# Kernel optimization log

Measured on AMD Instinct MI355X. Metric: run time of the kernel, lower is better.

## Reference

```python
import jax, jax.numpy as jnp
import numpy as np

M_LOCAL = 100000
N_GLOBAL = 50000
C = 128
E = 1600000
EDGE_DIM = 16
BN_EPS = 1e-5


def setup_inputs() -> dict:
    key = jax.random.key(0)
    ks = jax.random.split(key, 12)
    s = 1.0 / np.sqrt(C)
    inp = {
        "h_local": jax.random.normal(ks[0], (M_LOCAL, C), jnp.float32),
        "h_global": jax.random.normal(ks[1], (N_GLOBAL, C), jnp.float32),
        "ea_flat": jax.random.normal(ks[2], (E, EDGE_DIM), jnp.float32),
        # GIN MLP: Linear(C,C) -> ReLU -> Linear(C,C)
        "W1": jax.random.normal(ks[3], (C, C), jnp.float32) * s,
        "b1": jnp.zeros((C,), jnp.float32),
        "W2": jax.random.normal(ks[4], (C, C), jnp.float32) * s,
        "b2": jnp.zeros((C,), jnp.float32),
        "eps": jnp.zeros((), jnp.float32),  # GIN train_eps, init 0
        "gamma_l": jnp.ones((C,), jnp.float32),
        "beta_l": jnp.zeros((C,), jnp.float32),
        "gamma_g": jnp.ones((C,), jnp.float32),
        "beta_g": jnp.zeros((C,), jnp.float32),
        "intra_ei": jax.random.randint(ks[5], (2, E), 0, M_LOCAL, jnp.int32),
        "node_ids": jax.random.randint(ks[6], (M_LOCAL,), 0, N_GLOBAL, jnp.int32),
        "valid": jnp.ones((M_LOCAL,), jnp.bool_),
        "N_total": N_GLOBAL,
    }
    return inp


def _batchnorm(x, gamma, beta):
    # training-mode BN: biased batch statistics over node dim
    mu = jnp.mean(x, axis=0)
    var = jnp.mean((x - mu) ** 2, axis=0)
    return (x - mu) * jax.lax.rsqrt(var + BN_EPS) * gamma + beta


def reference(h_local, h_global, ea_flat, W1, b1, W2, b2, eps,
              gamma_l, beta_l, gamma_g, beta_g,
              intra_ei, node_ids, valid, N_total):
    M = h_local.shape[0]
    valid_f = valid.astype(h_local.dtype)[:, None]
    clamped = jnp.maximum(node_ids, 0)

    # inject global context, zero padding
    h_in = (h_local + h_global[clamped]) * valid_f

    # GINConv: mlp((1+eps)*x + sum_{j->i} x_j)   (ea_flat unused for 'gin')
    src, dst = intra_ei[0], intra_ei[1]
    agg = jax.ops.segment_sum(h_in[src], dst, num_segments=M)
    pre = (1.0 + eps) * h_in + agg
    h_local_new = jnp.maximum(pre @ W1 + b1, 0.0) @ W2 + b2
    h_local_new = h_local_new * valid_f

    # cross-subgraph consensus: scatter mean into global nodes
    h_sum = jax.ops.segment_sum(h_local_new, clamped, num_segments=N_total)
    v_cnt = jax.ops.segment_sum(valid_f[:, 0], clamped, num_segments=N_total)
    h_global_new = h_sum / jnp.maximum(v_cnt, 1.0)[:, None]

    # local track: BN + residual (Identity since in==out) + mask (dropout p=0)
    h_local_new = _batchnorm(h_local_new, gamma_l, beta_l) + h_local
    h_local_new = h_local_new * valid_f

    # global track: BN + residual
    h_global_new = _batchnorm(h_global_new, gamma_g, beta_g) + h_global

    return (h_local_new, h_global_new)
```

## Files before the change

kernel.cpp:

```cpp
#include <hip/hip_runtime.h>

#define CDIM 128
#define BROWS 128
#define HROWS 64
#define SMAX2 2048
#define CHUNK 16384
#define PBLK 1024

typedef __bf16 bf16x8 __attribute__((ext_vector_type(8)));
typedef __bf16 bf16x4 __attribute__((ext_vector_type(4)));
typedef float f32x4 __attribute__((ext_vector_type(4)));

__global__ __launch_bounds__(256) void k_init(
    const float* __restrict__ hl, const float* __restrict__ hg,
    const int* __restrict__ nid, __bf16* __restrict__ h_in, int M)
{
    int idx = blockIdx.x * 256 + threadIdx.x;
    if (idx >= M * 16) return;
    int i = idx >> 4, q8 = idx & 15;
    int g = max(nid[i], 0);
    const float4* hl4 = reinterpret_cast<const float4*>(hl);
    const float4* hg4 = reinterpret_cast<const float4*>(hg);
    float4 a0 = hl4[i * 32 + q8 * 2], a1 = hl4[i * 32 + q8 * 2 + 1];
    float4 b0 = hg4[g * 32 + q8 * 2], b1 = hg4[g * 32 + q8 * 2 + 1];
    bf16x8 o;
    o[0] = (__bf16)(a0.x + b0.x); o[1] = (__bf16)(a0.y + b0.y);
    o[2] = (__bf16)(a0.z + b0.z); o[3] = (__bf16)(a0.w + b0.w);
    o[4] = (__bf16)(a1.x + b1.x); o[5] = (__bf16)(a1.y + b1.y);
    o[6] = (__bf16)(a1.z + b1.z); o[7] = (__bf16)(a1.w + b1.w);
    *reinterpret_cast<bf16x8*>(&h_in[(size_t)i * CDIM + q8 * 8]) = o;
}

__global__ __launch_bounds__(256) void k_count(
    const int* __restrict__ ei, const int* __restrict__ nid,
    int* __restrict__ bcnt, int* __restrict__ deg_g, int E, int M)
{
    __shared__ int lh[1024];
    int t = threadIdx.x;
    for (int i = t; i < 1024; i += 256) lh[i] = 0;
    __syncthreads();
    int stride = gridDim.x * 256;
    for (int e = blockIdx.x * 256 + t; e < E; e += stride)
        atomicAdd(&lh[ei[E + e] >> 7], 1);
    for (int i = blockIdx.x * 256 + t; i < M; i += stride)
        atomicAdd(&deg_g[max(nid[i], 0)], 1);
    __syncthreads();
    for (int i = t; i < 1024; i += 256)
        if (lh[i]) atomicAdd(&bcnt[i], lh[i]);
}

__global__ __launch_bounds__(1024) void k_scanA(
    const int* __restrict__ deg_g, int* __restrict__ bsum_g, int N, int nbN,
    const int* __restrict__ bcnt, int* __restrict__ bboff,
    int* __restrict__ bcur, int NB)
{
    __shared__ int sh[1024];
    int t = threadIdx.x;
    if ((int)blockIdx.x < nbN) {
        int i = blockIdx.x * 1024 + t;
        sh[t] = (i < N) ? deg_g[i] : 0;
        __syncthreads();
        for (int s = 512; s > 0; s >>= 1) {
            if (t < s) sh[t] += sh[t + s];
            __syncthreads();
        }
        if (t == 0) bsum_g[blockIdx.x] = sh[0];
    } else {
        int v = (t < NB) ? bcnt[t] : 0;
        sh[t] = v;
        __syncthreads();
        for (int s = 1; s < 1024; s <<= 1) {
            int a = (t >= s) ? sh[t - s] : 0;
            __syncthreads();
            sh[t] += a;
            __syncthreads();
        }
        if (t < NB) { int ex = sh[t] - v; bboff[t] = ex; bcur[t] = ex; }
        if (t == 0) bboff[NB] = sh[1023];
    }
}

__global__ __launch_bounds__(256) void k_scanB(int* __restrict__ bsum, int nb)
{
    __shared__ int sh[256];
    int t = threadIdx.x;
    int v = (t < nb) ? bsum[t] : 0;
    sh[t] = v;
    __syncthreads();
    for (int s = 1; s < 256; s <<= 1) {
        int a = (t >= s) ? sh[t - s] : 0;
        __syncthreads();
        sh[t] += a;
        __syncthreads();
    }
    if (t < nb) bsum[t] = sh[t] - v;
}

__global__ __launch_bounds__(1024) void k_scanC(
    const int* __restrict__ deg_g, const int* __restrict__ bsum_g,
    int* __restrict__ off_g, int N)
{
    __shared__ int sh[1024];
    int i = blockIdx.x * 1024 + threadIdx.x;
    int v = (i < N) ? deg_g[i] : 0;
    sh[threadIdx.x] = v;
    __syncthreads();
    for (int s = 1; s < 1024; s <<= 1) {
        int a = (threadIdx.x >= (unsigned)s) ? sh[threadIdx.x - s] : 0;
        __syncthreads();
        sh[threadIdx.x] += a;
        __syncthreads();
    }
    if (i < N) off_g[i] = bsum_g[blockIdx.x] + sh[threadIdx.x] - v;
}

__global__ __launch_bounds__(256) void k_bscatter(
    const int* __restrict__ ei, const int* __restrict__ nid,
    int* __restrict__ bcur, int* __restrict__ packed,
    const int* __restrict__ off_g, int* __restrict__ cur_g,
    int* __restrict__ rows_g, int E, int M)
{
    __shared__ int lh[1024];
    int t = threadIdx.x;
    int e0 = blockIdx.x * CHUNK;
    int n = min(CHUNK, E - e0);
    for (int i = t; i < 1024; i += 256) lh[i] = 0;
    __syncthreads();
    for (int j = t; j < n; j += 256)
        atomicAdd(&lh[ei[E + e0 + j] >> 7], 1);
    __syncthreads();
    for (int i = t; i < 1024; i += 256) {
        int c = lh[i];
        if (c) lh[i] = atomicAdd(&bcur[i], c);
    }
    __syncthreads();
    for (int j = t; j < n; j += 256) {
        int s = ei[e0 + j], d = ei[E + e0 + j];
        int pos = atomicAdd(&lh[d >> 7], 1);
        packed[pos] = s | ((d & 127) << 17);
    }
    for (int i = blockIdx.x * 256 + t; i < M; i += gridDim.x * 256) {
        int g = max(nid[i], 0);
        int pos = off_g[g] + atomicAdd(&cur_g[g], 1);
        rows_g[pos] = i;
    }
}

__global__ __launch_bounds__(256) void k_agg_fused(
    const __bf16* __restrict__ h_in, const int* __restrict__ packed,
    const int* __restrict__ bboff, const float* __restrict__ epsp,
    __bf16* __restrict__ pre, int M)
{
    __shared__ int lsrc[SMAX2];
    __shared__ int lcnt[HROWS], lbase[HROWS], lpos[HROWS];
    int t = threadIdx.x;
    int b = blockIdx.x >> 1;
    int half = blockIdx.x & 1;
    int base = bboff[b];
    int n = bboff[b + 1] - base;
    if (t < HROWS) lcnt[t] = 0;
    __syncthreads();
    for (int j = t; j < n; j += 256) {
        int ld = packed[base + j] >> 17;
        if ((ld >> 6) == half) atomicAdd(&lcnt[ld & 63], 1);
    }
    __syncthreads();
    int v = (t < HROWS) ? lcnt[t] : 0;
    if (t < HROWS) lbase[t] = v;
    __syncthreads();
    for (int s = 1; s < HROWS; s <<= 1) {
        int a = (t < HROWS && t >= s) ? lbase[t - s] : 0;
        __syncthreads();
        if (t < HROWS) lbase[t] += a;
        __syncthreads();
    }
    if (t < HROWS) { lbase[t] -= v; lpos[t] = lbase[t]; }
    __syncthreads();
    for (int j = t; j < n; j += 256) {
        int p = packed[base + j];
        int ld = p >> 17;
        if ((ld >> 6) == half) {
            int r = atomicAdd(&lpos[ld & 63], 1);
            if (r < SMAX2) lsrc[r] = p & 0x1FFFF;
        }
    }
    __syncthreads();

    float es = 1.0f + epsp[0];
    int slot = t >> 4, q = t & 15;
    int r0 = b * BROWS + half * HROWS;
    for (int rr = slot; rr < HROWS; rr += 16) {
        int row = r0 + rr;
        if (row >= M) break;
        bf16x8 a = *reinterpret_cast<const bf16x8*>(&h_in[(size_t)row * CDIM + q * 8]);
        float f[8];
#pragma unroll
        for (int k2 = 0; k2 < 8; ++k2) f[k2] = es * (float)a[k2];
        int sb = lbase[rr], cnt = lcnt[rr];
        for (int j = 0; j < cnt; ++j) {
            int s = lsrc[sb + j];
            bf16x8 vv = *reinterpret_cast<const bf16x8*>(&h_in[(size_t)s * CDIM + q * 8]);
#pragma unroll
            for (int k2 = 0; k2 < 8; ++k2) f[k2] += (float)vv[k2];
        }
        bf16x8 o;
#pragma unroll
        for (int k2 = 0; k2 < 8; ++k2) o[k2] = (__bf16)f[k2];
        *reinterpret_cast<bf16x8*>(&pre[(size_t)row * CDIM + q * 8]) = o;
    }
}

__global__ __launch_bounds__(256) void k_wprep(
    const float* __restrict__ W1, const float* __restrict__ W2,
    __bf16* __restrict__ Wt1, __bf16* __restrict__ Wt2)
{
    int idx = blockIdx.x * 256 + threadIdx.x;
    int k = idx >> 7, n = idx & 127;
    Wt1[n * CDIM + k] = (__bf16)W1[k * CDIM + n];
    Wt2[n * CDIM + k] = (__bf16)W2[k * CDIM + n];
}

template <int RELU>
__global__ __launch_bounds__(256) void k_gemm_mfma(
    const __bf16* __restrict__ A, const __bf16* __restrict__ Wt,
    const float* __restrict__ bias, __bf16* __restrict__ out, int M)
{
    __shared__ bf16x8 w_lds4[2048];
    int t = threadIdx.x;
#pragma unroll
    for (int j = 0; j < 8; ++j) {
        int c = t + j * 256;
        int n = c >> 4;
        int cr = c & 15;
        int kc = cr >> 2;
        int g = cr & 3;
        int dest = ((n >> 4) * 4 + kc) * 64 + g * 16 + (n & 15);
        w_lds4[dest] = reinterpret_cast<const bf16x8*>(Wt)[c];
    }
    __syncthreads();

    int wave = t >> 6, lane = t & 63;
    int r0 = blockIdx.x * 64 + wave * 16;
    int arow = r0 + (lane & 15);
    int srcrow = min(arow, M - 1);
    int krow = (lane >> 4) * 8;

    bf16x8 a[4];
#pragma unroll
    for (int kc = 0; kc < 4; ++kc)
        a[kc] = *reinterpret_cast<const bf16x8*>(
            &A[(size_t)srcrow * CDIM + kc * 32 + krow]);

    f32x4 acc[8] = {};
#pragma unroll
    for (int kc = 0; kc < 4; ++kc) {
#pragma unroll
        for (int nt = 0; nt < 8; ++nt) {
            bf16x8 b = w_lds4[(nt * 4 + kc) * 64 + lane];
            acc[nt] = __builtin_amdgcn_mfma_f32_16x16x32_bf16(a[kc], b, acc[nt], 0, 0, 0);
        }
    }

    int col = lane & 15;
    int rowbase = r0 + (lane >> 4) * 4;
#pragma unroll
    for (int nt = 0; nt < 8; ++nt) {
        float bv = bias[nt * 16 + col];
#pragma unroll
        for (int reg = 0; reg < 4; ++reg) {
            int row = rowbase + reg;
            if (row >= M) continue;
            float v = acc[nt][reg] + bv;
            if (RELU) v = fmaxf(v, 0.f);
            out[(size_t)row * CDIM + nt * 16 + col] = (__bf16)v;
        }
    }
}

__global__ __launch_bounds__(256) void k_gmean(
    const __bf16* __restrict__ y, const int* __restrict__ off,
    const int* __restrict__ deg, const int* __restrict__ rows,
    float* __restrict__ out_g, float* __restrict__ part, int N)
{
    int t = threadIdx.x;
    int q = t & 31;
    float4 csum = make_float4(0.f, 0.f, 0.f, 0.f);
    float4 csq  = make_float4(0.f, 0.f, 0.f, 0.f);
    for (int g = blockIdx.x * 8 + (t >> 5); g < N; g += gridDim.x * 8) {
        int s0 = off[g], n = deg[g];
        float4 acc = make_float4(0.f, 0.f, 0.f, 0.f);
        for (int j = 0; j < n; ++j) {
            int r = rows[s0 + j];
            bf16x4 v = *reinterpret_cast<const bf16x4*>(&y[(size_t)r * CDIM + q * 4]);
            acc.x += (float)v[0]; acc.y += (float)v[1];
            acc.z += (float)v[2]; acc.w += (float)v[3];
        }
        float inv = 1.0f / fmaxf((float)n, 1.0f);
        float4 m = make_float4(acc.x * inv, acc.y * inv, acc.z * inv, acc.w * inv);
        reinterpret_cast<float4*>(out_g)[(size_t)g * 32 + q] = m;
        csum.x += m.x; csum.y += m.y; csum.z += m.z; csum.w += m.w;
        csq.x = fmaf(m.x, m.x, csq.x); csq.y = fmaf(m.y, m.y, csq.y);
        csq.z = fmaf(m.z, m.z, csq.z); csq.w = fmaf(m.w, m.w, csq.w);
    }
    __shared__ float4 red[256];
    float* pb = part + (size_t)blockIdx.x * 256;
    red[t] = csum;
    __syncthreads();
    if (t < 32) {
        float4 a = red[t];
#pragma unroll
        for (int g = 1; g < 8; ++g) {
            float4 b = red[g * 32 + t];
            a.x += b.x; a.y += b.y; a.z += b.z; a.w += b.w;
        }
        reinterpret_cast<float4*>(pb)[t] = a;
    }
    __syncthreads();
    red[t] = csq;
    __syncthreads();
    if (t < 32) {
        float4 a = red[t];
#pragma unroll
        for (int g = 1; g < 8; ++g) {
            float4 b = red[g * 32 + t];
            a.x += b.x; a.y += b.y; a.z += b.z; a.w += b.w;
        }
        reinterpret_cast<float4*>(pb + 128)[t] = a;
    }
}

__global__ __launch_bounds__(256) void k_stats_y(
    const __bf16* __restrict__ y, float* __restrict__ part, int M)
{
    int t = threadIdx.x;
    int q = t & 31;
    float4 csum = make_float4(0.f, 0.f, 0.f, 0.f);
    float4 csq  = make_float4(0.f, 0.f, 0.f, 0.f);
    for (int p = blockIdx.x * 8 + (t >> 5); p < M; p += gridDim.x * 8) {
        bf16x4 v = *reinterpret_cast<const bf16x4*>(&y[(size_t)p * CDIM + q * 4]);
        float a = (float)v[0], b = (float)v[1], c = (float)v[2], d = (float)v[3];
        csum.x += a; csum.y += b; csum.z += c; csum.w += d;
        csq.x = fmaf(a, a, csq.x); csq.y = fmaf(b, b, csq.y);
        csq.z = fmaf(c, c, csq.z); csq.w = fmaf(d, d, csq.w);
    }
    __shared__ float4 red[256];
    float* pb = part + (size_t)blockIdx.x * 256;
    red[t] = csum;
    __syncthreads();
    if (t < 32) {
        float4 a = red[t];
#pragma unroll
        for (int g = 1; g < 8; ++g) {
            float4 b = red[g * 32 + t];
            a.x += b.x; a.y += b.y; a.z += b.z; a.w += b.w;
        }
        reinterpret_cast<float4*>(pb)[t] = a;
    }
    __syncthreads();
    red[t] = csq;
    __syncthreads();
    if (t < 32) {
        float4 a = red[t];
#pragma unroll
        for (int g = 1; g < 8; ++g) {
            float4 b = red[g * 32 + t];
            a.x += b.x; a.y += b.y; a.z += b.z; a.w += b.w;
        }
        reinterpret_cast<float4*>(pb + 128)[t] = a;
    }
}

__global__ __launch_bounds__(256) void k_reduce(
    const float* __restrict__ part_l, const float* __restrict__ part_g,
    float* __restrict__ stats)
{
    int r = blockIdx.x;
    const float* part = (r < 256) ? part_l : part_g;
    int col = r & 255;
    int t = threadIdx.x;
    float s = 0.f;
#pragma unroll
    for (int j = 0; j < PBLK / 256; ++j)
        s += part[(size_t)(t + j * 256) * 256 + col];
    __shared__ float sh[256];
    sh[t] = s;
    __syncthreads();
    for (int w = 128; w > 0; w >>= 1) {
        if (t < w) sh[t] += sh[t + w];
        __syncthreads();
    }
    if (t == 0) stats[(r < 256 ? 0 : 256) + col] = sh[0];
}

__global__ void k_scale(
    const float* __restrict__ stats, const float* __restrict__ gl,
    const float* __restrict__ bl, const float* __restrict__ gg,
    const float* __restrict__ bg, float* __restrict__ sc, int M, int N)
{
    int t = threadIdx.x;
    if (t < 128) {
        float invM = 1.0f / (float)M;
        float mu = stats[t] * invM;
        float var = stats[128 + t] * invM - mu * mu;
        float s = gl[t] * rsqrtf(var + 1e-5f);
        sc[t] = s;
        sc[128 + t] = bl[t] - mu * s;
    } else if (t < 256) {
        int c = t - 128;
        float invN = 1.0f / (float)N;
        float mu = stats[256 + c] * invN;
        float var = stats[384 + c] * invN - mu * mu;
        float s = gg[c] * rsqrtf(var + 1e-5f);
        sc[256 + c] = s;
        sc[384 + c] = bg[c] - mu * s;
    }
}

__global__ __launch_bounds__(256) void k_fin_l(
    const __bf16* __restrict__ y, const float* __restrict__ res,
    const float* __restrict__ sc, float* __restrict__ out_l, int M)
{
    int idx = blockIdx.x * 256 + threadIdx.x;
    if (idx >= M * 32) return;
    int q = idx & 31;
    float4 s4 = reinterpret_cast<const float4*>(sc)[q];
    float4 h4 = reinterpret_cast<const float4*>(sc + 128)[q];
    bf16x4 v = *reinterpret_cast<const bf16x4*>(&y[(size_t)idx * 4]);
    float4 r = reinterpret_cast<const float4*>(res)[idx];
    reinterpret_cast<float4*>(out_l)[idx] = make_float4(
        fmaf((float)v[0], s4.x, h4.x) + r.x, fmaf((float)v[1], s4.y, h4.y) + r.y,
        fmaf((float)v[2], s4.z, h4.z) + r.z, fmaf((float)v[3], s4.w, h4.w) + r.w);
}

__global__ __launch_bounds__(256) void k_fin_g(
    float* __restrict__ X, const float* __restrict__ res,
    const float* __restrict__ sc, int rows)
{
    int idx = blockIdx.x * 256 + threadIdx.x;
    if (idx >= rows * 32) return;
    int q = idx & 31;
    float4 s4 = reinterpret_cast<const float4*>(sc)[q];
    float4 h4 = reinterpret_cast<const float4*>(sc + 128)[q];
    float4 v = reinterpret_cast<float4*>(X)[idx];
    float4 r = reinterpret_cast<const float4*>(res)[idx];
    reinterpret_cast<float4*>(X)[idx] = make_float4(
        fmaf(v.x, s4.x, h4.x) + r.x, fmaf(v.y, s4.y, h4.y) + r.y,
        fmaf(v.z, s4.z, h4.z) + r.z, fmaf(v.w, s4.w, h4.w) + r.w);
}

extern "C" void kernel_launch(void* const* d_in, const int* in_sizes, int n_in,
                              void* d_out, int out_size, void* d_ws, size_t ws_size,
                              hipStream_t stream)
{
    const float* h_local  = (const float*)d_in[0];
    const float* h_global = (const float*)d_in[1];
    const float* W1   = (const float*)d_in[3];
    const float* b1   = (const float*)d_in[4];
    const float* W2   = (const float*)d_in[5];
    const float* b2   = (const float*)d_in[6];
    const float* eps  = (const float*)d_in[7];
    const float* gl   = (const float*)d_in[8];
    const float* bl   = (const float*)d_in[9];
    const float* gg   = (const float*)d_in[10];
    const float* bg   = (const float*)d_in[11];
    const int*   ei   = (const int*)d_in[12];
    const int*   nid  = (const int*)d_in[13];

    const int M = in_sizes[13];
    const int N = in_sizes[1] / CDIM;
    const int E = in_sizes[12] / 2;
    const int NB = (M + BROWS - 1) / BROWS;

    float* out_l = (float*)d_out;
    float* out_g = out_l + (size_t)M * CDIM;

    __bf16* pre = (__bf16*)d_out;

    int* deg_g  = (int*)((char*)d_out + 26000000);
    int* cur_g  = deg_g + N;
    int* off_g  = cur_g + N;
    int* rows_g = off_g + N;
    int* bsum_g = rows_g + M;

    float* part_l = (float*)((char*)d_out + 28000000);
    float* part_g = part_l + (size_t)PBLK * 256;

    int* packed = (int*)out_g;

    __bf16* h_in = (__bf16*)d_ws;
    __bf16* h1   = h_in;
    __bf16* y    = (__bf16*)((char*)d_ws + 25600000);
    char*  wst   = (char*)d_ws + 51200000;
    __bf16* Wt1  = (__bf16*)wst;
    __bf16* Wt2  = Wt1 + CDIM * CDIM;
    int*   bcnt  = (int*)(Wt2 + CDIM * CDIM);
    int*   bboff = bcnt + 1024;
    int*   bcur  = bboff + 1024;
    float* stats = (float*)(bcur + 1024);
    float* sc    = stats + 512;

    const int nbN = (N + 1023) / 1024;

    hipMemsetAsync(deg_g, 0, (size_t)2 * N * sizeof(int), stream);
    hipMemsetAsync(bcnt, 0, 1024 * sizeof(int), stream);

    k_wprep<<<64, 256, 0, stream>>>(W1, W2, Wt1, Wt2);

    int gInit = (M * 16 + 255) / 256;
    k_init<<<gInit, 256, 0, stream>>>(h_local, h_global, nid, h_in, M);

    k_count<<<256, 256, 0, stream>>>(ei, nid, bcnt, deg_g, E, M);
    k_scanA<<<nbN + 1, 1024, 0, stream>>>(deg_g, bsum_g, N, nbN, bcnt, bboff, bcur, NB);
    k_scanB<<<1, 256, 0, stream>>>(bsum_g, nbN);
    k_scanC<<<nbN, 1024, 0, stream>>>(deg_g, bsum_g, off_g, N);

    int gBS = (E + CHUNK - 1) / CHUNK;
    k_bscatter<<<gBS, 256, 0, stream>>>(ei, nid, bcur, packed,
                                        off_g, cur_g, rows_g, E, M);

    k_agg_fused<<<NB * 2, 256, 0, stream>>>(h_in, packed, bboff, eps, pre, M);

    int gGemm = (M + 63) / 64;
    k_gemm_mfma<1><<<gGemm, 256, 0, stream>>>(pre, Wt1, b1, h1, M);
    k_gemm_mfma<0><<<gGemm, 256, 0, stream>>>(h1, Wt2, b2, y, M);

    k_gmean<<<PBLK, 256, 0, stream>>>(y, off_g, deg_g, rows_g, out_g, part_g, N);
    k_stats_y<<<PBLK, 256, 0, stream>>>(y, part_l, M);
    k_reduce<<<512, 256, 0, stream>>>(part_l, part_g, stats);

    k_scale<<<1, 256, 0, stream>>>(stats, gl, bl, gg, bg, sc, M, N);

    int gFinL = (M * 32 + 255) / 256;
    k_fin_l<<<gFinL, 256, 0, stream>>>(y, h_local, sc, out_l, M);
    int gFinG = (N * 32 + 255) / 256;
    k_fin_g<<<gFinG, 256, 0, stream>>>(out_g, h_global, sc + 256, N);
}
```

Baseline: 275.0 us.

## Fuse both MLP GEMMs and BN statistics into one kernel, split aggregation finer

The two MFMA GEMM launches become a single k_mlp kernel. The ReLU'd hidden tile stays in LDS and the second weight matrix is reloaded into the same LDS buffer. Per-column sum and sum-of-squares for the local BatchNorm are gathered in the GEMM epilogue through shuffles and LDS atomics, which removes the separate k_stats_y pass over y and the global round trip of h1. The neighbour aggregation now splits each 128-row bucket into quarters instead of halves, with a smaller LDS source list, and unrolls the gather loop by two. The gmean grid is also enlarged. Risks: the smaller per-quarter LDS list (1024) could overflow on high-degree buckets, and the fused kernel's larger LDS footprint may lower occupancy.

```diff
diff --git a/kernel.cpp b/kernel.cpp
--- a/kernel.cpp
+++ b/kernel.cpp
@@ -2,10 +2,11 @@
 
 #define CDIM 128
 #define BROWS 128
-#define HROWS 64
-#define SMAX2 2048
+#define QROWS 32
+#define SMAXQ 1024
 #define CHUNK 16384
-#define PBLK 1024
+#define GMB 2048
+#define H1LD 136
 
 typedef __bf16 bf16x8 __attribute__((ext_vector_type(8)));
 typedef __bf16 bf16x4 __attribute__((ext_vector_type(4)));
@@ -151,45 +152,47 @@
     const int* __restrict__ bboff, const float* __restrict__ epsp,
     __bf16* __restrict__ pre, int M)
 {
-    __shared__ int lsrc[SMAX2];
-    __shared__ int lcnt[HROWS], lbase[HROWS], lpos[HROWS];
-    int t = threadIdx.x;
-    int b = blockIdx.x >> 1;
-    int half = blockIdx.x & 1;
+    __shared__ int lsrc[SMAXQ];
+    __shared__ int lcnt[QROWS], lbase[QROWS], lpos[QROWS];
+    int t = threadIdx.x;
+    int b = blockIdx.x >> 2;
+    int quarter = blockIdx.x & 3;
     int base = bboff[b];
     int n = bboff[b + 1] - base;
-    if (t < HROWS) lcnt[t] = 0;
+    if (t < QROWS) lcnt[t] = 0;
     __syncthreads();
     for (int j = t; j < n; j += 256) {
         int ld = packed[base + j] >> 17;
-        if ((ld >> 6) == half) atomicAdd(&lcnt[ld & 63], 1);
-    }
-    __syncthreads();
-    int v = (t < HROWS) ? lcnt[t] : 0;
-    if (t < HROWS) lbase[t] = v;
-    __syncthreads();
-    for (int s = 1; s < HROWS; s <<= 1) {
-        int a = (t < HROWS && t >= s) ? lbase[t - s] : 0;
-        __syncthreads();
-        if (t < HROWS) lbase[t] += a;
-        __syncthreads();
-    }
-    if (t < HROWS) { lbase[t] -= v; lpos[t] = lbase[t]; }
+        if ((ld >> 5) == quarter) atomicAdd(&lcnt[ld & 31], 1);
+    }
+    __syncthreads();
+    int v = (t < QROWS) ? lcnt[t] : 0;
+    if (t < QROWS) lbase[t] = v;
+    __syncthreads();
+    for (int s = 1; s < QROWS; s <<= 1) {
+        int a = (t < QROWS && t >= s) ? lbase[t - s] : 0;
+        __syncthreads();
+        if (t < QROWS) lbase[t] += a;
+        __syncthreads();
+    }
+    if (t < QROWS) { lbase[t] -= v; lpos[t] = lbase[t]; }
     __syncthreads();
     for (int j = t; j < n; j += 256) {
         int p = packed[base + j];
         int ld = p >> 17;
-        if ((ld >> 6) == half) {
-            int r = atomicAdd(&lpos[ld & 63], 1);
-            if (r < SMAX2) lsrc[r] = p & 0x1FFFF;
+        if ((ld >> 5) == quarter) {
+            int r = atomicAdd(&lpos[ld & 31], 1);
+            if (r < SMAXQ) lsrc[r] = p & 0x1FFFF;
         }
     }
     __syncthreads();
 
     float es = 1.0f + epsp[0];
     int slot = t >> 4, q = t & 15;
-    int r0 = b * BROWS + half * HROWS;
-    for (int rr = slot; rr < HROWS; rr += 16) {
+    int r0 = b * BROWS + quarter * QROWS;
+#pragma unroll
+    for (int rr0 = 0; rr0 < 2; ++rr0) {
+        int rr = slot + rr0 * 16;
         int row = r0 + rr;
         if (row >= M) break;
         bf16x8 a = *reinterpret_cast<const bf16x8*>(&h_in[(size_t)row * CDIM + q * 8]);
@@ -197,11 +200,19 @@
 #pragma unroll
         for (int k2 = 0; k2 < 8; ++k2) f[k2] = es * (float)a[k2];
         int sb = lbase[rr], cnt = lcnt[rr];
-        for (int j = 0; j < cnt; ++j) {
-            int s = lsrc[sb + j];
-            bf16x8 vv = *reinterpret_cast<const bf16x8*>(&h_in[(size_t)s * CDIM + q * 8]);
-#pragma unroll
-            for (int k2 = 0; k2 < 8; ++k2) f[k2] += (float)vv[k2];
+        int j = 0;
+        for (; j + 1 < cnt; j += 2) {
+            int s0 = lsrc[sb + j], s1 = lsrc[sb + j + 1];
+            bf16x8 v0 = *reinterpret_cast<const bf16x8*>(&h_in[(size_t)s0 * CDIM + q * 8]);
+            bf16x8 v1 = *reinterpret_cast<const bf16x8*>(&h_in[(size_t)s1 * CDIM + q * 8]);
+#pragma unroll
+            for (int k2 = 0; k2 < 8; ++k2) f[k2] += (float)v0[k2] + (float)v1[k2];
+        }
+        if (j < cnt) {
+            int s0 = lsrc[sb + j];
+            bf16x8 v0 = *reinterpret_cast<const bf16x8*>(&h_in[(size_t)s0 * CDIM + q * 8]);
+#pragma unroll
+            for (int k2 = 0; k2 < 8; ++k2) f[k2] += (float)v0[k2];
         }
         bf16x8 o;
 #pragma unroll
@@ -220,61 +231,105 @@
     Wt2[n * CDIM + k] = (__bf16)W2[k * CDIM + n];
 }
 
-template <int RELU>
-__global__ __launch_bounds__(256) void k_gemm_mfma(
-    const __bf16* __restrict__ A, const __bf16* __restrict__ Wt,
-    const float* __restrict__ bias, __bf16* __restrict__ out, int M)
+__global__ __launch_bounds__(256) void k_mlp(
+    const __bf16* __restrict__ pre, const __bf16* __restrict__ Wt1,
+    const __bf16* __restrict__ Wt2, const float* __restrict__ b1,
+    const float* __restrict__ b2, __bf16* __restrict__ y,
+    float* __restrict__ part, int M)
 {
     __shared__ bf16x8 w_lds4[2048];
+    __shared__ __bf16 h1t[64 * H1LD];
+    __shared__ float pst[256];
     int t = threadIdx.x;
 #pragma unroll
     for (int j = 0; j < 8; ++j) {
         int c = t + j * 256;
-        int n = c >> 4;
-        int cr = c & 15;
-        int kc = cr >> 2;
-        int g = cr & 3;
-        int dest = ((n >> 4) * 4 + kc) * 64 + g * 16 + (n & 15);
-        w_lds4[dest] = reinterpret_cast<const bf16x8*>(Wt)[c];
-    }
+        int n = c >> 4, cr = c & 15, kc = cr >> 2, g = cr & 3;
+        w_lds4[((n >> 4) * 4 + kc) * 64 + g * 16 + (n & 15)] =
+            reinterpret_cast<const bf16x8*>(Wt1)[c];
+    }
+    if (t < 256) pst[t] = 0.f;
     __syncthreads();
 
     int wave = t >> 6, lane = t & 63;
     int r0 = blockIdx.x * 64 + wave * 16;
-    int arow = r0 + (lane & 15);
-    int srcrow = min(arow, M - 1);
+    int srcrow = min(r0 + (lane & 15), M - 1);
     int krow = (lane >> 4) * 8;
+    int col = lane & 15;
 
     bf16x8 a[4];
 #pragma unroll
     for (int kc = 0; kc < 4; ++kc)
         a[kc] = *reinterpret_cast<const bf16x8*>(
-            &A[(size_t)srcrow * CDIM + kc * 32 + krow]);
-
-    f32x4 acc[8] = {};
-#pragma unroll
-    for (int kc = 0; kc < 4; ++kc) {
-#pragma unroll
-        for (int nt = 0; nt < 8; ++nt) {
-            bf16x8 b = w_lds4[(nt * 4 + kc) * 64 + lane];
-            acc[nt] = __builtin_amdgcn_mfma_f32_16x16x32_bf16(a[kc], b, acc[nt], 0, 0, 0);
-        }
-    }
-
-    int col = lane & 15;
+            &pre[(size_t)srcrow * CDIM + kc * 32 + krow]);
+
+    f32x4 acc1[8] = {};
+#pragma unroll
+    for (int kc = 0; kc < 4; ++kc)
+#pragma unroll
+        for (int nt = 0; nt < 8; ++nt)
+            acc1[nt] = __builtin_amdgcn_mfma_f32_16x16x32_bf16(
+                a[kc], w_lds4[(nt * 4 + kc) * 64 + lane], acc1[nt], 0, 0, 0);
+
+    int lrowb = wave * 16 + (lane >> 4) * 4;
+#pragma unroll
+    for (int nt = 0; nt < 8; ++nt) {
+        float bv = b1[nt * 16 + col];
+#pragma unroll
+        for (int reg = 0; reg < 4; ++reg) {
+            float v = fmaxf(acc1[nt][reg] + bv, 0.f);
+            h1t[(lrowb + reg) * H1LD + nt * 16 + col] = (__bf16)v;
+        }
+    }
+    __syncthreads();
+
+#pragma unroll
+    for (int j = 0; j < 8; ++j) {
+        int c = t + j * 256;
+        int n = c >> 4, cr = c & 15, kc = cr >> 2, g = cr & 3;
+        w_lds4[((n >> 4) * 4 + kc) * 64 + g * 16 + (n & 15)] =
+            reinterpret_cast<const bf16x8*>(Wt2)[c];
+    }
+    __syncthreads();
+
+    int lrow = wave * 16 + (lane & 15);
+    bf16x8 a2[4];
+#pragma unroll
+    for (int kc = 0; kc < 4; ++kc)
+        a2[kc] = *reinterpret_cast<const bf16x8*>(&h1t[lrow * H1LD + kc * 32 + krow]);
+
+    f32x4 acc2[8] = {};
+#pragma unroll
+    for (int kc = 0; kc < 4; ++kc)
+#pragma unroll
+        for (int nt = 0; nt < 8; ++nt)
+            acc2[nt] = __builtin_amdgcn_mfma_f32_16x16x32_bf16(
+                a2[kc], w_lds4[(nt * 4 + kc) * 64 + lane], acc2[nt], 0, 0, 0);
+
     int rowbase = r0 + (lane >> 4) * 4;
 #pragma unroll
     for (int nt = 0; nt < 8; ++nt) {
-        float bv = bias[nt * 16 + col];
+        float bv = b2[nt * 16 + col];
+        float s = 0.f, s2 = 0.f;
 #pragma unroll
         for (int reg = 0; reg < 4; ++reg) {
             int row = rowbase + reg;
-            if (row >= M) continue;
-            float v = acc[nt][reg] + bv;
-            if (RELU) v = fmaxf(v, 0.f);
-            out[(size_t)row * CDIM + nt * 16 + col] = (__bf16)v;
-        }
-    }
+            float v = acc2[nt][reg] + bv;
+            if (row < M) {
+                y[(size_t)row * CDIM + nt * 16 + col] = (__bf16)v;
+                s += v;
+                s2 = fmaf(v, v, s2);
+            }
+        }
+        s += __shfl_xor(s, 16); s += __shfl_xor(s, 32);
+        s2 += __shfl_xor(s2, 16); s2 += __shfl_xor(s2, 32);
+        if ((lane >> 4) == 0) {
+            atomicAdd(&pst[nt * 16 + col], s);
+            atomicAdd(&pst[128 + nt * 16 + col], s2);
+        }
+    }
+    __syncthreads();
+    if (t < 256) part[(size_t)blockIdx.x * 256 + t] = pst[t];
 }
 
 __global__ __launch_bounds__(256) void k_gmean(
@@ -329,59 +384,18 @@
     }
 }
 
-__global__ __launch_bounds__(256) void k_stats_y(
-    const __bf16* __restrict__ y, float* __restrict__ part, int M)
-{
-    int t = threadIdx.x;
-    int q = t & 31;
-    float4 csum = make_float4(0.f, 0.f, 0.f, 0.f);
-    float4 csq  = make_float4(0.f, 0.f, 0.f, 0.f);
-    for (int p = blockIdx.x * 8 + (t >> 5); p < M; p += gridDim.x * 8) {
-        bf16x4 v = *reinterpret_cast<const bf16x4*>(&y[(size_t)p * CDIM + q * 4]);
-        float a = (float)v[0], b = (float)v[1], c = (float)v[2], d = (float)v[3];
-        csum.x += a; csum.y += b; csum.z += c; csum.w += d;
-        csq.x = fmaf(a, a, csq.x); csq.y = fmaf(b, b, csq.y);
-        csq.z = fmaf(c, c, csq.z); csq.w = fmaf(d, d, csq.w);
-    }
-    __shared__ float4 red[256];
-    float* pb = part + (size_t)blockIdx.x * 256;
-    red[t] = csum;
-    __syncthreads();
-    if (t < 32) {
-        float4 a = red[t];
-#pragma unroll
-        for (int g = 1; g < 8; ++g) {
-            float4 b = red[g * 32 + t];
-            a.x += b.x; a.y += b.y; a.z += b.z; a.w += b.w;
-        }
-        reinterpret_cast<float4*>(pb)[t] = a;
-    }
-    __syncthreads();
-    red[t] = csq;
-    __syncthreads();
-    if (t < 32) {
-        float4 a = red[t];
-#pragma unroll
-        for (int g = 1; g < 8; ++g) {
-            float4 b = red[g * 32 + t];
-            a.x += b.x; a.y += b.y; a.z += b.z; a.w += b.w;
-        }
-        reinterpret_cast<float4*>(pb + 128)[t] = a;
-    }
-}
-
 __global__ __launch_bounds__(256) void k_reduce(
-    const float* __restrict__ part_l, const float* __restrict__ part_g,
-    float* __restrict__ stats)
+    const float* __restrict__ part_l, int nl,
+    const float* __restrict__ part_g, int ng, float* __restrict__ stats)
 {
     int r = blockIdx.x;
     const float* part = (r < 256) ? part_l : part_g;
+    int n = (r < 256) ? nl : ng;
     int col = r & 255;
     int t = threadIdx.x;
     float s = 0.f;
-#pragma unroll
-    for (int j = 0; j < PBLK / 256; ++j)
-        s += part[(size_t)(t + j * 256) * 256 + col];
+    for (int i = t; i < n; i += 256)
+        s += part[(size_t)i * 256 + col];
     __shared__ float sh[256];
     sh[t] = s;
     __syncthreads();
@@ -470,6 +484,7 @@
     const int N = in_sizes[1] / CDIM;
     const int E = in_sizes[12] / 2;
     const int NB = (M + BROWS - 1) / BROWS;
+    const int gGemm = (M + 63) / 64;
 
     float* out_l = (float*)d_out;
     float* out_g = out_l + (size_t)M * CDIM;
@@ -483,12 +498,11 @@
     int* bsum_g = rows_g + M;
 
     float* part_l = (float*)((char*)d_out + 28000000);
-    float* part_g = part_l + (size_t)PBLK * 256;
+    float* part_g = part_l + (size_t)gGemm * 256;
 
     int* packed = (int*)out_g;
 
     __bf16* h_in = (__bf16*)d_ws;
-    __bf16* h1   = h_in;
     __bf16* y    = (__bf16*)((char*)d_ws + 25600000);
     char*  wst   = (char*)d_ws + 51200000;
     __bf16* Wt1  = (__bf16*)wst;
@@ -518,15 +532,12 @@
     k_bscatter<<<gBS, 256, 0, stream>>>(ei, nid, bcur, packed,
                                         off_g, cur_g, rows_g, E, M);
 
-    k_agg_fused<<<NB * 2, 256, 0, stream>>>(h_in, packed, bboff, eps, pre, M);
-
-    int gGemm = (M + 63) / 64;
-    k_gemm_mfma<1><<<gGemm, 256, 0, stream>>>(pre, Wt1, b1, h1, M);
-    k_gemm_mfma<0><<<gGemm, 256, 0, stream>>>(h1, Wt2, b2, y, M);
-
-    k_gmean<<<PBLK, 256, 0, stream>>>(y, off_g, deg_g, rows_g, out_g, part_g, N);
-    k_stats_y<<<PBLK, 256, 0, stream>>>(y, part_l, M);
-    k_reduce<<<512, 256, 0, stream>>>(part_l, part_g, stats);
+    k_agg_fused<<<NB * 4, 256, 0, stream>>>(h_in, packed, bboff, eps, pre, M);
+
+    k_mlp<<<gGemm, 256, 0, stream>>>(pre, Wt1, Wt2, b1, b2, y, part_l, M);
+
+    k_gmean<<<GMB, 256, 0, stream>>>(y, off_g, deg_g, rows_g, out_g, part_g, N);
+    k_reduce<<<512, 256, 0, stream>>>(part_l, gGemm, part_g, GMB, stats);
 
     k_scale<<<1, 256, 0, stream>>>(stats, gl, bl, gg, bg, sc, M, N);
 
```

After: 267.3 us. 2.8% less time.
